# Kernel optimization log

Hardware: AMD Instinct MI355X
Metric: run time of the kernel (lower is better)

The kernel has to match this reference:

```python
import jax, jax.numpy as jnp
import numpy as np
from jax import lax

HID = 20      # MDRNN2D hidden size
CIN = 10      # channels out of conv1
NG = 5        # gates: i, f_up, f_left, g, o


def _mdlstm_dir(x, Wx, Whu, Whl, bg):
    """One scan direction of a 2D MD-LSTM over grid x: [B,H,W,CIN].
    Cell (i,j) receives hidden/cell state from (i-1,j) and (i,j-1),
    with separate forget gates for each predecessor.
    Returns hidden map [B,HID,H,W]."""
    B, H, W, _ = x.shape
    # precompute input contribution to all gates: [H,W,B,5*HID]
    gx = jnp.einsum('bhwc,cg->hwbg', x, Wx) + bg
    h0 = jnp.zeros((W, B, HID), x.dtype)
    c0 = jnp.zeros((W, B, HID), x.dtype)

    def row_step(carry, gx_row):
        h_up, c_up = carry  # previous row states: [W,B,HID]

        def col_step(cc, inp):
            h_l, c_l = cc          # left neighbor: [B,HID]
            g_x, h_u, c_u = inp    # [B,5H], [B,HID], [B,HID]
            g = g_x + h_u @ Whu + h_l @ Whl
            i, f1, f2, z, o = jnp.split(g, NG, axis=-1)
            i = jax.nn.sigmoid(i)
            f1 = jax.nn.sigmoid(f1)
            f2 = jax.nn.sigmoid(f2)
            o = jax.nn.sigmoid(o)
            z = jnp.tanh(z)
            c = f1 * c_u + f2 * c_l + i * z
            h = o * jnp.tanh(c)
            return (h, c), (h, c)

        init = (jnp.zeros((gx_row.shape[1], HID), gx_row.dtype),
                jnp.zeros((gx_row.shape[1], HID), gx_row.dtype))
        _, (h_row, c_row) = lax.scan(col_step, init, (gx_row, h_up, c_up))
        return (h_row, c_row), h_row  # h_row: [W,B,HID]

    _, hs = lax.scan(row_step, (h0, c0), gx)     # [H,W,B,HID]
    return jnp.transpose(hs, (2, 3, 0, 1))       # [B,HID,H,W]


def setup_inputs() -> dict:
    key = jax.random.key(0)
    ks = jax.random.split(key, 9)
    s = 0.1
    B = 2048
    return {
        'x': jax.random.normal(ks[0], (B, 3, 32, 32), jnp.float32),
        'conv_w': jax.random.normal(ks[1], (CIN, 3, 3, 3), jnp.float32) * s,
        'conv_b': jax.random.normal(ks[2], (CIN,), jnp.float32) * s,
        'Wx': jax.random.normal(ks[3], (4, CIN, NG * HID), jnp.float32) * s,
        'Whu': jax.random.normal(ks[4], (4, HID, NG * HID), jnp.float32) * s,
        'Whl': jax.random.normal(ks[5], (4, HID, NG * HID), jnp.float32) * s,
        'bg': jax.random.normal(ks[6], (4, NG * HID), jnp.float32) * s,
        'fc_w': jax.random.normal(ks[7], (4 * HID, 10), jnp.float32) * s,
        'fc_b': jax.random.normal(ks[8], (10,), jnp.float32) * s,
    }


def reference(x, conv_w, conv_b, Wx, Whu, Whl, bg, fc_w, fc_b):
    # conv1: Conv2d(3,10,k=3,p=0) -> MaxPool(2,2) -> Tanh
    y = lax.conv_general_dilated(x, conv_w, (1, 1), 'VALID',
                                 dimension_numbers=('NCHW', 'OIHW', 'NCHW'))
    y = y + conv_b[None, :, None, None]                       # [B,10,30,30]
    y = lax.reduce_window(y, -jnp.inf, lax.max,
                          (1, 1, 2, 2), (1, 1, 2, 2), 'VALID')  # [B,10,15,15]
    y = jnp.tanh(y)
    feat = jnp.transpose(y, (0, 2, 3, 1))                     # [B,15,15,10]

    # 4 scan directions via spatial flips: origins TL, BL, TR, BR
    flips = [(False, False), (True, False), (False, True), (True, True)]
    outs = []
    for d, (fh, fw) in enumerate(flips):
        xi = feat
        if fh:
            xi = xi[:, ::-1]
        if fw:
            xi = xi[:, :, ::-1]
        h = _mdlstm_dir(xi, Wx[d], Whu[d], Whl[d], bg[d])      # [B,HID,H,W]
        if fh:
            h = h[:, :, ::-1]
        if fw:
            h = h[:, :, :, ::-1]
        outs.append(h)
    om = jnp.stack(outs, axis=2)                              # [B,HID,4,H,W]

    # corner readout per direction (final accumulated state of each scan)
    f1 = om[:, :, 0, -1, -1]
    f2 = om[:, :, 1, 0, -1]
    f3 = om[:, :, 2, -1, 0]
    f4 = om[:, :, 3, 0, 0]
    feats = jnp.concatenate([f1, f2, f3, f4], axis=1)         # [B,80]
    return feats @ fc_w + fc_b                                # [B,10]
```

## Files before the change

kernel.cpp:

```cpp
#include <hip/hip_runtime.h>
#include <math.h>

#define NB 2048
#define CINC 10
#define HID 20
#define NG 5
#define GDIM 100
#define GH 15
#define GW 15
#define BW 3

typedef _Float16 half2v __attribute__((ext_vector_type(2)));
typedef _Float16 half4v __attribute__((ext_vector_type(4)));
typedef _Float16 half8v __attribute__((ext_vector_type(8)));

#if defined(__has_builtin)
#if __has_builtin(__builtin_amdgcn_fdot2)
#define HAVE_FDOT2 1
#endif
#endif

__device__ __forceinline__ float fdot2f(half2v a, half2v b, float c) {
#ifdef HAVE_FDOT2
    return __builtin_amdgcn_fdot2(a, b, c, false);
#else
    return c + (float)a[0] * (float)b[0] + (float)a[1] * (float)b[1];
#endif
}

__device__ __forceinline__ float sigf(float x) {
    return __builtin_amdgcn_rcpf(1.f + __expf(-x));
}
__device__ __forceinline__ float tanhfast(float x) {
    float ax = fabsf(x);
    float e = __expf(-2.f * ax);
    float t = (1.f - e) * __builtin_amdgcn_rcpf(1.f + e);
    return copysignf(t, x);
}

#define SV8(v, a, b) ((half2v)__builtin_shufflevector(v, v, a, b))
#define SV4(v, a, b) ((half2v)__builtin_shufflevector(v, v, a, b))

__global__ __launch_bounds__(256) void conv_pool_tanh(
    const float* __restrict__ x,
    const float* __restrict__ conv_w,
    const float* __restrict__ conv_b,
    half2v* __restrict__ featH)
{
    __shared__ float wl[270];
    __shared__ float bl[10];
    int tid = threadIdx.x;
    for (int e = tid; e < 270; e += 256) wl[e] = conv_w[e];
    if (tid < 10) bl[tid] = conv_b[tid];
    __syncthreads();
    int gid = blockIdx.x * 256 + tid;
    if (gid >= NB * 225) return;
    int b = gid / 225;
    int r = gid % 225;
    int i = r / 15, j = r % 15;
    const float* xb = x + (size_t)b * 3 * 1024;

    float win[3][4][4];
    #pragma unroll
    for (int ic = 0; ic < 3; ++ic)
        #pragma unroll
        for (int rr = 0; rr < 4; ++rr)
            #pragma unroll
            for (int cc = 0; cc < 4; ++cc)
                win[ic][rr][cc] = xb[ic * 1024 + (2 * i + rr) * 32 + (2 * j + cc)];

    float vals[10];
    #pragma unroll
    for (int oc = 0; oc < CINC; ++oc) {
        float a00, a01, a10, a11;
        a00 = a01 = a10 = a11 = bl[oc];
        #pragma unroll
        for (int ic = 0; ic < 3; ++ic)
            #pragma unroll
            for (int kr = 0; kr < 3; ++kr)
                #pragma unroll
                for (int kc = 0; kc < 3; ++kc) {
                    float w = wl[(oc * 3 + ic) * 9 + kr * 3 + kc];
                    a00 += win[ic][kr][kc]         * w;
                    a01 += win[ic][kr][kc + 1]     * w;
                    a10 += win[ic][kr + 1][kc]     * w;
                    a11 += win[ic][kr + 1][kc + 1] * w;
                }
        float m = fmaxf(fmaxf(a00, a01), fmaxf(a10, a11));
        vals[oc] = tanhfast(m);
    }
    half2v* fo = featH + (size_t)gid * 6;
    half2v w0; w0[0] = (_Float16)vals[0]; w0[1] = (_Float16)vals[1]; fo[0] = w0;
    half2v w1; w1[0] = (_Float16)vals[2]; w1[1] = (_Float16)vals[3]; fo[1] = w1;
    half2v w2; w2[0] = (_Float16)vals[4]; w2[1] = (_Float16)0.f;     fo[2] = w2;
    half2v w3; w3[0] = (_Float16)vals[5]; w3[1] = (_Float16)vals[6]; fo[3] = w3;
    half2v w4; w4[0] = (_Float16)vals[7]; w4[1] = (_Float16)vals[8]; fo[4] = w4;
    half2v w5; w5[0] = (_Float16)vals[9]; w5[1] = (_Float16)0.f;     fo[5] = w5;
}

__global__ __launch_bounds__(64) void mdlstm_scan(
    const _Float16* __restrict__ featF,
    const float* __restrict__ Wx,
    const float* __restrict__ Whu,
    const float* __restrict__ Whl,
    const float* __restrict__ bg,
    float* __restrict__ corners)
{
    int t = threadIdx.x;
    int b = t / HID;
    int j = t % HID;
    bool act = (t < BW * HID);
    int bl = act ? b : 0;
    int d = blockIdx.y;
    int bglob = blockIdx.x * BW + b;
    bool bval = act && (bglob < NB);
    int fh = (d == 1 || d == 3);
    int fw = (d == 2 || d == 3);

    half2v wU[10][NG], wL[10][NG], wX2[6][NG];
    {
        const float* WU = Whu + d * HID * GDIM;
        const float* WL = Whl + d * HID * GDIM;
        #pragma unroll
        for (int m = 0; m < 10; ++m)
            #pragma unroll
            for (int g = 0; g < NG; ++g) {
                int cidx = g * HID + j;
                half2v w; w[0] = (_Float16)WU[(2*m)*GDIM + cidx]; w[1] = (_Float16)WU[(2*m+1)*GDIM + cidx];
                wU[m][g] = w;
                half2v v; v[0] = (_Float16)WL[(2*m)*GDIM + cidx]; v[1] = (_Float16)WL[(2*m+1)*GDIM + cidx];
                wL[m][g] = v;
            }
        const int cha[6] = {0, 2, 4, 5, 7, 9};
        const int chb[6] = {1, 3, -1, 6, 8, -1};
        const float* WXp = Wx + d * CINC * GDIM;
        #pragma unroll
        for (int w = 0; w < 6; ++w)
            #pragma unroll
            for (int g = 0; g < NG; ++g) {
                int cidx = g * HID + j;
                half2v v;
                v[0] = (_Float16)WXp[cha[w] * GDIM + cidx];
                v[1] = (chb[w] >= 0) ? (_Float16)WXp[chb[w] * GDIM + cidx] : (_Float16)0.f;
                wX2[w][g] = v;
            }
    }
    float bgr[NG];
    #pragma unroll
    for (int g = 0; g < NG; ++g) bgr[g] = bg[d * GDIM + g * HID + j];

    __shared__ _Float16 hR[2][GW + 1][BW][24];
    __shared__ float    cR[GW][BW][HID];
    __shared__ _Float16 fr[GW][BW][16];

    for (int e = t; e < 2 * (GW + 1) * BW * 24; e += 64) (&hR[0][0][0][0])[e] = (_Float16)0.f;
    for (int e = t; e < GW * BW * HID; e += 64) (&cR[0][0][0])[e] = 0.f;

    for (int i = 0; i < GH; ++i) {
        int p = i & 1, q = p ^ 1;
        int fi = fh ? (GH - 1 - i) : i;
        for (int e = t; e < GW * BW * 6; e += 64) {
            int col = e / (BW * 6);
            int rem = e % (BW * 6);
            int bb  = rem / 6;
            int w   = rem % 6;
            int bs  = blockIdx.x * BW + bb; if (bs >= NB) bs = NB - 1;
            int fcol = fw ? (GW - 1 - col) : col;
            ((unsigned*)fr)[(col * BW + bb) * 8 + w] =
                ((const unsigned*)featF)[((size_t)bs * 225 + fi * 15 + fcol) * 6 + w];
        }
        float cl = 0.f;

        #pragma unroll 5
        for (int jc = 0; jc < GW; ++jc) {
            const _Float16* hu_p = &hR[q][jc + 1][bl][0];
            const _Float16* hl_p = &hR[p][jc][bl][0];
            half8v u0 = *(const half8v*)(hu_p);
            half8v u1 = *(const half8v*)(hu_p + 8);
            half4v u2 = *(const half4v*)(hu_p + 16);
            half8v l0 = *(const half8v*)(hl_p);
            half8v l1 = *(const half8v*)(hl_p + 8);
            half4v l2 = *(const half4v*)(hl_p + 16);
            half8v x0 = *(const half8v*)&fr[jc][bl][0];
            half4v x1 = *(const half4v*)&fr[jc][bl][8];
            float cu = cR[jc][bl][j];

            half2v up[10] = { SV8(u0,0,1), SV8(u0,2,3), SV8(u0,4,5), SV8(u0,6,7),
                              SV8(u1,0,1), SV8(u1,2,3), SV8(u1,4,5), SV8(u1,6,7),
                              SV4(u2,0,1), SV4(u2,2,3) };
            half2v lf[10] = { SV8(l0,0,1), SV8(l0,2,3), SV8(l0,4,5), SV8(l0,6,7),
                              SV8(l1,0,1), SV8(l1,2,3), SV8(l1,4,5), SV8(l1,6,7),
                              SV4(l2,0,1), SV4(l2,2,3) };
            half2v xp[6]  = { SV8(x0,0,1), SV8(x0,2,3), SV8(x0,4,5), SV8(x0,6,7),
                              SV4(x1,0,1), SV4(x1,2,3) };

            float acc[NG];
            #pragma unroll
            for (int g = 0; g < NG; ++g) acc[g] = bgr[g];
            #pragma unroll
            for (int m = 0; m < 10; ++m)
                #pragma unroll
                for (int g = 0; g < NG; ++g) acc[g] = fdot2f(up[m], wU[m][g], acc[g]);
            #pragma unroll
            for (int m = 0; m < 10; ++m)
                #pragma unroll
                for (int g = 0; g < NG; ++g) acc[g] = fdot2f(lf[m], wL[m][g], acc[g]);
            #pragma unroll
            for (int w = 0; w < 6; ++w)
                #pragma unroll
                for (int g = 0; g < NG; ++g) acc[g] = fdot2f(xp[w], wX2[w][g], acc[g]);

            float gi = sigf(acc[0]);
            float g1 = sigf(acc[1]);
            float g2 = sigf(acc[2]);
            float zz = tanhfast(acc[3]);
            float go = sigf(acc[4]);
            float cn = g1 * cu + g2 * cl + gi * zz;
            float hn = go * tanhfast(cn);

            if (act) {
                hR[p][jc + 1][bl][j] = (_Float16)hn;
                cR[jc][bl][j] = cn;
            }
            cl = cn;
            if (bval && i == GH - 1 && jc == GW - 1)
                corners[(size_t)bglob * 80 + d * HID + j] = hn;
        }
    }
}

__global__ __launch_bounds__(256) void fc_kernel(
    const float* __restrict__ corners,
    const float* __restrict__ fc_w,
    const float* __restrict__ fc_b,
    float* __restrict__ out)
{
    __shared__ float w[800];
    __shared__ float bb[10];
    int t = threadIdx.x;
    for (int e = t; e < 800; e += 256) w[e] = fc_w[e];
    if (t < 10) bb[t] = fc_b[t];
    __syncthreads();
    int gid = blockIdx.x * 256 + t;
    if (gid >= NB * 10) return;
    int b = gid / 10, o = gid % 10;
    float acc = bb[o];
    #pragma unroll 8
    for (int k = 0; k < 80; ++k)
        acc += corners[(size_t)b * 80 + k] * w[k * 10 + o];
    out[gid] = acc;
}

extern "C" void kernel_launch(void* const* d_in, const int* in_sizes, int n_in,
                              void* d_out, int out_size, void* d_ws, size_t ws_size,
                              hipStream_t stream) {
    const float* x      = (const float*)d_in[0];
    const float* conv_w = (const float*)d_in[1];
    const float* conv_b = (const float*)d_in[2];
    const float* Wx     = (const float*)d_in[3];
    const float* Whu    = (const float*)d_in[4];
    const float* Whl    = (const float*)d_in[5];
    const float* bg     = (const float*)d_in[6];
    const float* fc_w   = (const float*)d_in[7];
    const float* fc_b   = (const float*)d_in[8];
    float* out = (float*)d_out;

    half2v*    featH = (half2v*)d_ws;
    _Float16*  featF = (_Float16*)d_ws;
    float* corners   = (float*)d_ws + (size_t)NB * 225 * 6;

    conv_pool_tanh<<<dim3((NB * 225 + 255) / 256), 256, 0, stream>>>(x, conv_w, conv_b, featH);
    mdlstm_scan<<<dim3((NB + BW - 1) / BW, 4), 64, 0, stream>>>(featF, Wx, Whu, Whl, bg, corners);
    fc_kernel<<<dim3((NB * 10 + 255) / 256), 256, 0, stream>>>(corners, fc_w, fc_b, out);
}
```

Measured before the change: 433.3 us.

## Process MD-LSTM rows in skewed pairs to interleave two independent cell chains

The scan now handles two grid rows per outer iteration. The second row runs two columns behind the first in the same loop, so each step computes two independent cells and exposes more instruction-level parallelism in a latency-bound recurrence. Feature loads are staged for both rows at once, the last odd row gets its own tail loop, and the cell math is factored into a macro. Launch bounds now request 3 waves per SIMD, which may cap registers and cause spills given the larger live set.

```diff
diff --git a/kernel.cpp b/kernel.cpp
--- a/kernel.cpp
+++ b/kernel.cpp
@@ -40,6 +40,46 @@
 
 #define SV8(v, a, b) ((half2v)__builtin_shufflevector(v, v, a, b))
 #define SV4(v, a, b) ((half2v)__builtin_shufflevector(v, v, a, b))
+
+#define CELL(HUP, HLP, FXP, CU, CLV, HN, CN) do {                                   \
+    const _Float16* hup_ = (HUP); const _Float16* hlp_ = (HLP);                     \
+    const _Float16* fxp_ = (FXP);                                                   \
+    half8v u0_ = *(const half8v*)(hup_);                                            \
+    half8v u1_ = *(const half8v*)(hup_ + 8);                                        \
+    half4v u2_ = *(const half4v*)(hup_ + 16);                                       \
+    half8v l0_ = *(const half8v*)(hlp_);                                            \
+    half8v l1_ = *(const half8v*)(hlp_ + 8);                                        \
+    half4v l2_ = *(const half4v*)(hlp_ + 16);                                       \
+    half8v x0_ = *(const half8v*)(fxp_);                                            \
+    half4v x1_ = *(const half4v*)(fxp_ + 8);                                        \
+    half2v up_[10] = { SV8(u0_,0,1),SV8(u0_,2,3),SV8(u0_,4,5),SV8(u0_,6,7),         \
+                       SV8(u1_,0,1),SV8(u1_,2,3),SV8(u1_,4,5),SV8(u1_,6,7),         \
+                       SV4(u2_,0,1),SV4(u2_,2,3) };                                 \
+    half2v lf_[10] = { SV8(l0_,0,1),SV8(l0_,2,3),SV8(l0_,4,5),SV8(l0_,6,7),         \
+                       SV8(l1_,0,1),SV8(l1_,2,3),SV8(l1_,4,5),SV8(l1_,6,7),         \
+                       SV4(l2_,0,1),SV4(l2_,2,3) };                                 \
+    half2v xp_[6]  = { SV8(x0_,0,1),SV8(x0_,2,3),SV8(x0_,4,5),SV8(x0_,6,7),         \
+                       SV4(x1_,0,1),SV4(x1_,2,3) };                                 \
+    float acc_[NG];                                                                 \
+    _Pragma("unroll") for (int g_ = 0; g_ < NG; ++g_) acc_[g_] = bgr[g_];           \
+    _Pragma("unroll") for (int m_ = 0; m_ < 10; ++m_) {                             \
+        _Pragma("unroll") for (int g_ = 0; g_ < NG; ++g_)                           \
+            acc_[g_] = fdot2f(up_[m_], wU[m_][g_], acc_[g_]); }                     \
+    _Pragma("unroll") for (int m_ = 0; m_ < 10; ++m_) {                             \
+        _Pragma("unroll") for (int g_ = 0; g_ < NG; ++g_)                           \
+            acc_[g_] = fdot2f(lf_[m_], wL[m_][g_], acc_[g_]); }                     \
+    _Pragma("unroll") for (int w_ = 0; w_ < 6; ++w_) {                              \
+        _Pragma("unroll") for (int g_ = 0; g_ < NG; ++g_)                           \
+            acc_[g_] = fdot2f(xp_[w_], wX2[w_][g_], acc_[g_]); }                    \
+    float gi_ = sigf(acc_[0]);                                                      \
+    float g1_ = sigf(acc_[1]);                                                      \
+    float g2_ = sigf(acc_[2]);                                                      \
+    float zz_ = tanhfast(acc_[3]);                                                  \
+    float go_ = sigf(acc_[4]);                                                      \
+    (CN) = g1_ * (CU) + g2_ * (CLV) + gi_ * zz_;                                    \
+    (HN) = go_ * tanhfast(CN);                                                      \
+    (CLV) = (CN);                                                                   \
+} while (0)
 
 __global__ __launch_bounds__(256) void conv_pool_tanh(
     const float* __restrict__ x,
@@ -98,7 +138,7 @@
     half2v w5; w5[0] = (_Float16)vals[9]; w5[1] = (_Float16)0.f;     fo[5] = w5;
 }
 
-__global__ __launch_bounds__(64) void mdlstm_scan(
+__global__ __launch_bounds__(64, 3) void mdlstm_scan(
     const _Float16* __restrict__ featF,
     const float* __restrict__ Wx,
     const float* __restrict__ Whu,
@@ -149,81 +189,83 @@
     #pragma unroll
     for (int g = 0; g < NG; ++g) bgr[g] = bg[d * GDIM + g * HID + j];
 
-    __shared__ _Float16 hR[2][GW + 1][BW][24];
-    __shared__ float    cR[GW][BW][HID];
-    __shared__ _Float16 fr[GW][BW][16];
-
-    for (int e = t; e < 2 * (GW + 1) * BW * 24; e += 64) (&hR[0][0][0][0])[e] = (_Float16)0.f;
-    for (int e = t; e < GW * BW * HID; e += 64) (&cR[0][0][0])[e] = 0.f;
-
-    for (int i = 0; i < GH; ++i) {
-        int p = i & 1, q = p ^ 1;
-        int fi = fh ? (GH - 1 - i) : i;
+    __shared__ _Float16 hBuf[2][GW + 1][BW][24];
+    __shared__ float    cBuf[GW][BW][HID];
+    __shared__ _Float16 fr[2][GW][BW][16];
+
+    for (int e = t; e < 2 * (GW + 1) * BW * 24; e += 64) (&hBuf[0][0][0][0])[e] = (_Float16)0.f;
+    for (int e = t; e < GW * BW * HID; e += 64) (&cBuf[0][0][0])[e] = 0.f;
+
+    int uv = 0;
+    for (int r = 0; r < 7; ++r) {
+        int i0 = 2 * r, i1 = 2 * r + 1;
+        {
+            int fi0 = fh ? (GH - 1 - i0) : i0;
+            int fi1 = fh ? (GH - 1 - i1) : i1;
+            for (int e = t; e < 2 * GW * BW * 6; e += 64) {
+                int fb  = e / (GW * BW * 6);
+                int rem = e % (GW * BW * 6);
+                int col = rem / (BW * 6);
+                int r2  = rem % (BW * 6);
+                int bb  = r2 / 6, w = r2 % 6;
+                int bs  = blockIdx.x * BW + bb; if (bs >= NB) bs = NB - 1;
+                int fcol = fw ? (GW - 1 - col) : col;
+                int fi  = fb ? fi1 : fi0;
+                ((unsigned*)fr)[(fb * GW * BW + col * BW + bb) * 8 + w] =
+                    ((const unsigned*)featF)[((size_t)bs * 225 + fi * 15 + fcol) * 6 + w];
+            }
+        }
+        _Float16* U = &hBuf[uv][0][0][0];
+        _Float16* V = &hBuf[uv ^ 1][0][0][0];
+        float clA = 0.f, clB = 0.f;
+        for (int tt = 0; tt < GW + 2; ++tt) {
+            if (tt < GW) {
+                float cu = cBuf[tt][bl][j];
+                float hn, cn;
+                CELL(U + ((tt + 1) * BW + bl) * 24,
+                     U + (tt * BW + bl) * 24,
+                     &fr[0][tt][bl][0], cu, clA, hn, cn);
+                if (act) {
+                    U[((tt + 1) * BW + bl) * 24 + j] = (_Float16)hn;
+                    cBuf[tt][bl][j] = cn;
+                }
+            }
+            if (tt >= 2) {
+                int u = tt - 2;
+                float cu = cBuf[u][bl][j];
+                float hn, cn;
+                CELL(U + ((u + 1) * BW + bl) * 24,
+                     V + (u * BW + bl) * 24,
+                     &fr[1][u][bl][0], cu, clB, hn, cn);
+                if (act) {
+                    V[((u + 1) * BW + bl) * 24 + j] = (_Float16)hn;
+                    cBuf[u][bl][j] = cn;
+                }
+            }
+        }
+        uv ^= 1;
+    }
+    {
+        int fi0 = fh ? 0 : (GH - 1);
         for (int e = t; e < GW * BW * 6; e += 64) {
             int col = e / (BW * 6);
-            int rem = e % (BW * 6);
-            int bb  = rem / 6;
-            int w   = rem % 6;
+            int r2  = e % (BW * 6);
+            int bb  = r2 / 6, w = r2 % 6;
             int bs  = blockIdx.x * BW + bb; if (bs >= NB) bs = NB - 1;
             int fcol = fw ? (GW - 1 - col) : col;
             ((unsigned*)fr)[(col * BW + bb) * 8 + w] =
-                ((const unsigned*)featF)[((size_t)bs * 225 + fi * 15 + fcol) * 6 + w];
+                ((const unsigned*)featF)[((size_t)bs * 225 + fi0 * 15 + fcol) * 6 + w];
         }
-        float cl = 0.f;
-
-        #pragma unroll 5
-        for (int jc = 0; jc < GW; ++jc) {
-            const _Float16* hu_p = &hR[q][jc + 1][bl][0];
-            const _Float16* hl_p = &hR[p][jc][bl][0];
-            half8v u0 = *(const half8v*)(hu_p);
-            half8v u1 = *(const half8v*)(hu_p + 8);
-            half4v u2 = *(const half4v*)(hu_p + 16);
-            half8v l0 = *(const half8v*)(hl_p);
-            half8v l1 = *(const half8v*)(hl_p + 8);
-            half4v l2 = *(const half4v*)(hl_p + 16);
-            half8v x0 = *(const half8v*)&fr[jc][bl][0];
-            half4v x1 = *(const half4v*)&fr[jc][bl][8];
-            float cu = cR[jc][bl][j];
-
-            half2v up[10] = { SV8(u0,0,1), SV8(u0,2,3), SV8(u0,4,5), SV8(u0,6,7),
-                              SV8(u1,0,1), SV8(u1,2,3), SV8(u1,4,5), SV8(u1,6,7),
-                              SV4(u2,0,1), SV4(u2,2,3) };
-            half2v lf[10] = { SV8(l0,0,1), SV8(l0,2,3), SV8(l0,4,5), SV8(l0,6,7),
-                              SV8(l1,0,1), SV8(l1,2,3), SV8(l1,4,5), SV8(l1,6,7),
-                              SV4(l2,0,1), SV4(l2,2,3) };
-            half2v xp[6]  = { SV8(x0,0,1), SV8(x0,2,3), SV8(x0,4,5), SV8(x0,6,7),
-                              SV4(x1,0,1), SV4(x1,2,3) };
-
-            float acc[NG];
-            #pragma unroll
-            for (int g = 0; g < NG; ++g) acc[g] = bgr[g];
-            #pragma unroll
-            for (int m = 0; m < 10; ++m)
-                #pragma unroll
-                for (int g = 0; g < NG; ++g) acc[g] = fdot2f(up[m], wU[m][g], acc[g]);
-            #pragma unroll
-            for (int m = 0; m < 10; ++m)
-                #pragma unroll
-                for (int g = 0; g < NG; ++g) acc[g] = fdot2f(lf[m], wL[m][g], acc[g]);
-            #pragma unroll
-            for (int w = 0; w < 6; ++w)
-                #pragma unroll
-                for (int g = 0; g < NG; ++g) acc[g] = fdot2f(xp[w], wX2[w][g], acc[g]);
-
-            float gi = sigf(acc[0]);
-            float g1 = sigf(acc[1]);
-            float g2 = sigf(acc[2]);
-            float zz = tanhfast(acc[3]);
-            float go = sigf(acc[4]);
-            float cn = g1 * cu + g2 * cl + gi * zz;
-            float hn = go * tanhfast(cn);
-
-            if (act) {
-                hR[p][jc + 1][bl][j] = (_Float16)hn;
-                cR[jc][bl][j] = cn;
-            }
-            cl = cn;
-            if (bval && i == GH - 1 && jc == GW - 1)
+        _Float16* U = &hBuf[uv][0][0][0];
+        float clA = 0.f;
+        for (int tt = 0; tt < GW; ++tt) {
+            float cu = cBuf[tt][bl][j];
+            float hn, cn;
+            CELL(U + ((tt + 1) * BW + bl) * 24,
+                 U + (tt * BW + bl) * 24,
+                 &fr[0][tt][bl][0], cu, clA, hn, cn);
+            if (act) U[((tt + 1) * BW + bl) * 24 + j] = (_Float16)hn;
+            if (bval && tt == GW - 1)
                 corners[(size_t)bglob * 80 + d * HID + j] = hn;
         }
     }
```

After: 553.0 us. 27.6% more time.
